# Performance work log

Measured on AMD Instinct MI355X. Metric: run time of the kernel, lower is better.

## Reference

```python
import jax, jax.numpy as jnp
import numpy as np

N_WG = 256                 # waveguides per side
N_TOTAL = N_WG * N_WG      # 65536 field points
NNZ = 16 * N_TOTAL         # ~16 couplings per waveguide (Knn-banded)
PROP_DIS = 1.0


def setup_inputs() -> dict:
    key = jax.random.key(0)
    k1, k2, k3, k4, k5 = jax.random.split(key, 5)
    row_idx = jax.random.randint(k1, (NNZ,), 0, N_TOTAL, dtype=jnp.int32)
    col_idx = jax.random.randint(k2, (NNZ,), 0, N_TOTAL, dtype=jnp.int32)
    # small coupling values so the explicit Euler scheme stays stable
    A_vals = jax.random.normal(k3, (NNZ,), dtype=jnp.float32) * 0.01
    Ur0 = jax.random.normal(k4, (N_TOTAL, 1), dtype=jnp.float32)
    Ui0 = jax.random.normal(k5, (N_TOTAL, 1), dtype=jnp.float32)
    return {"A_vals": A_vals, "row_idx": row_idx, "col_idx": col_idx,
            "Ur0": Ur0, "Ui0": Ui0, "Euler_steps": 16}


def reference(A_vals, row_idx, col_idx, Ur0, Ui0, Euler_steps):
    """Euler propagation of a complex field U under sparse coupling A:
       dU/dz = i * A @ U  ->  Ur' = Ur - dz*A@Ui ; Ui' = Ui + dz*A@Ur.
       Matches gen_Euler_with_backward_devs.forward (single device block)."""
    dz = PROP_DIS / Euler_steps

    def spmm(x):  # sparse COO matmul: [n, n] @ [n, 1]
        return jax.ops.segment_sum(A_vals[:, None] * x[col_idx], row_idx,
                                   num_segments=N_TOTAL)

    def step(carry, _):
        Ur, Ui = carry
        Ur1 = Ur - dz * spmm(Ui)
        Ui1 = Ui + dz * spmm(Ur)
        return (Ur1, Ui1), None

    (Ur, Ui), _ = jax.lax.scan(step, (Ur0, Ui0), None, length=Euler_steps)
    return Ur + 1j * Ui
```

## Files before the change

kernel.cpp:

```cpp
#include <hip/hip_runtime.h>

#define N_TOTAL 65536
#define NNZ (16 * N_TOTAL)
#define EULER_STEPS 16
#define SLOTS 48
#define TB 256
#define P 256
#define PROWS (N_TOTAL / P)
#define CHUNK 1024
#define NCHUNK (NNZ / CHUNK)
#define SCAP 24


__global__ __launch_bounds__(TB) void scatter_kernel(
    const float* __restrict__ A_vals, const int* __restrict__ row_idx,
    const int* __restrict__ col_idx, int* __restrict__ hist_t,
    uint2* __restrict__ staged) {
  __shared__ int cur[P];
  const int b = blockIdx.x, t = threadIdx.x;
  cur[t] = 0;
  __syncthreads();
  const int base = b * CHUNK;
  for (int i = t; i < CHUNK; i += TB) {
    int e = base + i;
    int r = row_idx[e];
    int p = r >> 8;
    int pos = atomicAdd(&cur[p], 1);
    if (pos < SCAP)
      staged[(size_t)(p * NCHUNK + b) * SCAP + pos] =
          make_uint2((unsigned)col_idx[e] | ((unsigned)(r & 255) << 16),
                     __float_as_uint(A_vals[e]));
  }
  __syncthreads();
  int c = cur[t];
  hist_t[t * NCHUNK + b] = (c > SCAP) ? SCAP : c;
}

__global__ __launch_bounds__(512) void build_step1_kernel(
    const uint2* __restrict__ staged, const int* __restrict__ hist_t,
    int* __restrict__ cntg, unsigned* __restrict__ entries,
    const float* __restrict__ Ur0, const float* __restrict__ Ui0,
    float2* __restrict__ Unew, float dz) {
  __shared__ unsigned ell[PROWS * SLOTS];
  __shared__ int cnt[PROWS];
  __shared__ int hcnt[NCHUNK];
  const int p = blockIdx.x, t = threadIdx.x;
  for (int i = t; i < NCHUNK; i += 512) hcnt[i] = hist_t[p * NCHUNK + i];
  for (int r = t; r < PROWS; r += 512) cnt[r] = 0;
  __syncthreads();
  for (int chunk = t; chunk < NCHUNK; chunk += 512) {
    int c = hcnt[chunk];
    const uint2* seg = staged + (size_t)(p * NCHUNK + chunk) * SCAP;
    for (int i = 0; i < c; ++i) {
      uint2 el = seg[i];
      int r = (el.x >> 16) & 255;
      int slot = atomicAdd(&cnt[r], 1);
      if (slot < SLOTS) {
        unsigned bv = el.y;
        unsigned rb = (bv + 0x7FFFu + ((bv >> 16) & 1u)) & 0xFFFF0000u;
        ell[r * SLOTS + slot] = (el.x & 0xFFFFu) | rb;
      }
    }
  }
  __syncthreads();
  const int rowbase = p * PROWS;
  for (int idx = t; idx < PROWS * SLOTS; idx += 512)
    entries[rowbase * SLOTS + idx] = ell[idx];
  for (int r = t; r < PROWS; r += 512) {
    int c = cnt[r];
    cntg[rowbase + r] = (c > SLOTS) ? SLOTS : c;
  }
  const int lr = t >> 1, l = t & 1;
  const int row = rowbase + lr;
  int c = cnt[lr];
  if (c > SLOTS) c = SLOTS;
  float sR = 0.0f, sI = 0.0f;
  for (int s = l; s < c; s += 2) {
    unsigned e = ell[lr * SLOTS + s];
    float a = __uint_as_float(e & 0xFFFF0000u);
    int col = (int)(e & 0xFFFFu);
    sR += a * Ur0[col];
    sI += a * Ui0[col];
  }
  sR += __shfl_xor(sR, 1);
  sI += __shfl_xor(sI, 1);
  if (l == 0)
    Unew[row] = make_float2(Ur0[row] - dz * sI, Ui0[row] + dz * sR);
}

__global__ __launch_bounds__(TB) void step_mid_kernel(
    const int* __restrict__ cnt, const unsigned* __restrict__ entries,
    const float2* __restrict__ Uold, float2* __restrict__ Unew, float dz) {
  int tid = blockIdx.x * blockDim.x + threadIdx.x;
  int row = tid >> 3, l = tid & 7;
  int c = cnt[row];
  if (c > SLOTS) c = SLOTS;
  const unsigned* base = entries + row * SLOTS;
  float sR = 0.0f, sI = 0.0f;
  for (int k = 2 * l; k < c; k += 16) {
    uint2 p = *(const uint2*)(base + k);
    {
      float a = __uint_as_float(p.x & 0xFFFF0000u);
      float2 u = Uold[p.x & 0xFFFFu];
      sR += a * u.x;
      sI += a * u.y;
    }
    if (k + 1 < c) {
      float a = __uint_as_float(p.y & 0xFFFF0000u);
      float2 u = Uold[p.y & 0xFFFFu];
      sR += a * u.x;
      sI += a * u.y;
    }
  }
  sR += __shfl_xor(sR, 1); sI += __shfl_xor(sI, 1);
  sR += __shfl_xor(sR, 2); sI += __shfl_xor(sI, 2);
  sR += __shfl_xor(sR, 4); sI += __shfl_xor(sI, 4);
  if (l == 0) {
    float2 u = Uold[row];
    Unew[row] = make_float2(u.x - dz * sI, u.y + dz * sR);
  }
}

__global__ __launch_bounds__(TB) void step_final_kernel(
    const int* __restrict__ cnt, const unsigned* __restrict__ entries,
    const float2* __restrict__ Uold, float* __restrict__ UrOut,
    float* __restrict__ UiOut, float dz) {
  int tid = blockIdx.x * blockDim.x + threadIdx.x;
  int row = tid >> 3, l = tid & 7;
  int c = cnt[row];
  if (c > SLOTS) c = SLOTS;
  const unsigned* base = entries + row * SLOTS;
  float sR = 0.0f, sI = 0.0f;
  for (int k = 2 * l; k < c; k += 16) {
    uint2 p = *(const uint2*)(base + k);
    {
      float a = __uint_as_float(p.x & 0xFFFF0000u);
      float2 u = Uold[p.x & 0xFFFFu];
      sR += a * u.x;
      sI += a * u.y;
    }
    if (k + 1 < c) {
      float a = __uint_as_float(p.y & 0xFFFF0000u);
      float2 u = Uold[p.y & 0xFFFFu];
      sR += a * u.x;
      sI += a * u.y;
    }
  }
  sR += __shfl_xor(sR, 1); sI += __shfl_xor(sI, 1);
  sR += __shfl_xor(sR, 2); sI += __shfl_xor(sI, 2);
  sR += __shfl_xor(sR, 4); sI += __shfl_xor(sI, 4);
  if (l == 0) {
    float2 u = Uold[row];
    UrOut[row] = u.x - dz * sI;
    UiOut[row] = u.y + dz * sR;
  }
}

extern "C" void kernel_launch(void* const* d_in, const int* in_sizes, int n_in,
                              void* d_out, int out_size, void* d_ws,
                              size_t ws_size, hipStream_t stream) {
  const float* A_vals  = (const float*)d_in[0];
  const int*   row_idx = (const int*)d_in[1];
  const int*   col_idx = (const int*)d_in[2];
  const float* Ur0     = (const float*)d_in[3];
  const float* Ui0     = (const float*)d_in[4];

  char* ws = (char*)d_ws;
  float2*   bufA    = (float2*)ws;
  float2*   bufB    = bufA + N_TOTAL;
  int*      cntg    = (int*)(bufB + N_TOTAL);
  unsigned* entries = (unsigned*)(cntg + N_TOTAL);
  int*      hist_t  = (int*)(entries + (size_t)N_TOTAL * SLOTS);
  uint2*    staged  = (uint2*)(hist_t + P * NCHUNK);

  float* UrOut = (float*)d_out;
  float* UiOut = UrOut + N_TOTAL;
  const float dz = 1.0f / (float)EULER_STEPS;
  const int gridN8 = (8 * N_TOTAL) / TB;

  scatter_kernel<<<NCHUNK, TB, 0, stream>>>(A_vals, row_idx, col_idx, hist_t,
                                            staged);
  build_step1_kernel<<<P, 512, 0, stream>>>(staged, hist_t, cntg, entries,
                                            Ur0, Ui0, bufB, dz);

  for (int s = 1; s < EULER_STEPS - 1; ++s) {
    const float2* src = (s & 1) ? bufB : bufA;
    float2*       dst = (s & 1) ? bufA : bufB;
    step_mid_kernel<<<gridN8, TB, 0, stream>>>(cntg, entries, src, dst, dz);
  }
  step_final_kernel<<<gridN8, TB, 0, stream>>>(cntg, entries, bufB, UrOut,
                                               UiOut, dz);
}
```

Measured before the change: 219.4 us.

## Fuse all stages into one persistent kernel with software grid barriers

```diff
diff --git a/kernel.cpp b/kernel.cpp
--- a/kernel.cpp
+++ b/kernel.cpp
@@ -4,53 +4,143 @@
 #define NNZ (16 * N_TOTAL)
 #define EULER_STEPS 16
 #define SLOTS 48
-#define TB 256
 #define P 256
-#define PROWS (N_TOTAL / P)
+#define PROWS 256
 #define CHUNK 1024
-#define NCHUNK (NNZ / CHUNK)
+#define NCHUNK 1024
 #define SCAP 24
 
-
-__global__ __launch_bounds__(TB) void scatter_kernel(
+#define TPB 1024
+#define NBLK 256
+#define CPB (NCHUNK / NBLK)
+#define NTHREADS (NBLK * TPB)
+#define NTASKS (8 * N_TOTAL)
+
+
+__device__ __forceinline__ float2 uload(const float2* p) {
+  unsigned long long d = __hip_atomic_load((const unsigned long long*)p,
+                                           __ATOMIC_RELAXED,
+                                           __HIP_MEMORY_SCOPE_AGENT);
+  float2 r;
+  r.x = __uint_as_float((unsigned)(d & 0xFFFFFFFFull));
+  r.y = __uint_as_float((unsigned)(d >> 32));
+  return r;
+}
+__device__ __forceinline__ void ustore(float2* p, float2 v) {
+  unsigned long long d = ((unsigned long long)__float_as_uint(v.y) << 32) |
+                         (unsigned long long)__float_as_uint(v.x);
+  __hip_atomic_store((unsigned long long*)p, d, __ATOMIC_RELAXED,
+                     __HIP_MEMORY_SCOPE_AGENT);
+}
+
+template <bool HEAVY>
+__device__ __forceinline__ void grid_barrier(int* bar) {
+  __syncthreads();
+  if (threadIdx.x == 0) {
+    if (HEAVY) __threadfence();
+    int* cnt = bar;
+    int* gen = bar + 16;
+    int g = __hip_atomic_load(gen, __ATOMIC_RELAXED, __HIP_MEMORY_SCOPE_AGENT);
+    int prev =
+        __hip_atomic_fetch_add(cnt, 1, __ATOMIC_RELAXED, __HIP_MEMORY_SCOPE_AGENT);
+    if (prev == (int)gridDim.x - 1) {
+      __hip_atomic_store(cnt, 0, __ATOMIC_RELAXED, __HIP_MEMORY_SCOPE_AGENT);
+      __hip_atomic_fetch_add(gen, 1, __ATOMIC_RELEASE, __HIP_MEMORY_SCOPE_AGENT);
+    } else {
+      while (__hip_atomic_load(gen, __ATOMIC_RELAXED,
+                               __HIP_MEMORY_SCOPE_AGENT) == g)
+        __builtin_amdgcn_s_sleep(8);
+    }
+    if (HEAVY) __threadfence();
+  }
+  __syncthreads();
+}
+
+template <bool FINAL>
+__device__ __forceinline__ void euler_step(const int* __restrict__ cntg,
+                                           const unsigned* __restrict__ entries,
+                                           const float2* __restrict__ src,
+                                           float2* __restrict__ dst,
+                                           float* __restrict__ UrOut,
+                                           float* __restrict__ UiOut, float dz,
+                                           int gtid) {
+#pragma unroll
+  for (int it = 0; it < NTASKS / NTHREADS; ++it) {
+    const int task = gtid + it * NTHREADS;
+    const int row = task >> 3;
+    const int l = task & 7;
+    const int c = cntg[row];
+    const unsigned* base = entries + row * SLOTS;
+    float sR = 0.0f, sI = 0.0f;
+    for (int k = 2 * l; k < c; k += 16) {
+      uint2 pr = *(const uint2*)(base + k);
+      {
+        float a = __uint_as_float(pr.x & 0xFFFF0000u);
+        float2 u = uload(&src[pr.x & 0xFFFFu]);
+        sR += a * u.x;
+        sI += a * u.y;
+      }
+      if (k + 1 < c) {
+        float a = __uint_as_float(pr.y & 0xFFFF0000u);
+        float2 u = uload(&src[pr.y & 0xFFFFu]);
+        sR += a * u.x;
+        sI += a * u.y;
+      }
+    }
+    sR += __shfl_xor(sR, 1); sI += __shfl_xor(sI, 1);
+    sR += __shfl_xor(sR, 2); sI += __shfl_xor(sI, 2);
+    sR += __shfl_xor(sR, 4); sI += __shfl_xor(sI, 4);
+    if (l == 0) {
+      float2 u = uload(&src[row]);
+      if (FINAL) {
+        UrOut[row] = u.x - dz * sI;
+        UiOut[row] = u.y + dz * sR;
+      } else {
+        ustore(&dst[row], make_float2(u.x - dz * sI, u.y + dz * sR));
+      }
+    }
+  }
+}
+
+__global__ __launch_bounds__(TPB, 4) void mega_kernel(
     const float* __restrict__ A_vals, const int* __restrict__ row_idx,
-    const int* __restrict__ col_idx, int* __restrict__ hist_t,
-    uint2* __restrict__ staged) {
-  __shared__ int cur[P];
-  const int b = blockIdx.x, t = threadIdx.x;
-  cur[t] = 0;
-  __syncthreads();
-  const int base = b * CHUNK;
-  for (int i = t; i < CHUNK; i += TB) {
-    int e = base + i;
-    int r = row_idx[e];
-    int p = r >> 8;
-    int pos = atomicAdd(&cur[p], 1);
-    if (pos < SCAP)
-      staged[(size_t)(p * NCHUNK + b) * SCAP + pos] =
-          make_uint2((unsigned)col_idx[e] | ((unsigned)(r & 255) << 16),
-                     __float_as_uint(A_vals[e]));
-  }
-  __syncthreads();
-  int c = cur[t];
-  hist_t[t * NCHUNK + b] = (c > SCAP) ? SCAP : c;
-}
-
-__global__ __launch_bounds__(512) void build_step1_kernel(
-    const uint2* __restrict__ staged, const int* __restrict__ hist_t,
-    int* __restrict__ cntg, unsigned* __restrict__ entries,
-    const float* __restrict__ Ur0, const float* __restrict__ Ui0,
-    float2* __restrict__ Unew, float dz) {
+    const int* __restrict__ col_idx, const float* __restrict__ Ur0,
+    const float* __restrict__ Ui0, int* __restrict__ cntg,
+    unsigned* __restrict__ entries, int* __restrict__ hist_t,
+    uint2* __restrict__ staged, float2* __restrict__ bufA,
+    float2* __restrict__ bufB, float* __restrict__ UrOut,
+    float* __restrict__ UiOut, int* bar, float dz) {
   __shared__ unsigned ell[PROWS * SLOTS];
   __shared__ int cnt[PROWS];
   __shared__ int hcnt[NCHUNK];
-  const int p = blockIdx.x, t = threadIdx.x;
-  for (int i = t; i < NCHUNK; i += 512) hcnt[i] = hist_t[p * NCHUNK + i];
-  for (int r = t; r < PROWS; r += 512) cnt[r] = 0;
-  __syncthreads();
-  for (int chunk = t; chunk < NCHUNK; chunk += 512) {
-    int c = hcnt[chunk];
-    const uint2* seg = staged + (size_t)(p * NCHUNK + chunk) * SCAP;
+  const int t = threadIdx.x;
+  const int b = blockIdx.x;
+  const int gtid = b * TPB + t;
+
+  for (int cidx = 0; cidx < CPB; ++cidx) {
+    const int chunk = b * CPB + cidx;
+    if (t < P) cnt[t] = 0;
+    __syncthreads();
+    const int e = chunk * CHUNK + t;
+    const int r = row_idx[e];
+    const int pp = r >> 8;
+    const int pos = atomicAdd(&cnt[pp], 1);
+    if (pos < SCAP)
+      staged[((size_t)pp * NCHUNK + chunk) * SCAP + pos] =
+          make_uint2((unsigned)col_idx[e] | ((unsigned)(r & 255) << 16),
+                     __float_as_uint(A_vals[e]));
+    __syncthreads();
+    if (t < P) hist_t[t * NCHUNK + chunk] = min(cnt[t], SCAP);
+    __syncthreads();
+  }
+  grid_barrier<true>(bar);
+
+  hcnt[t] = hist_t[b * NCHUNK + t];
+  if (t < PROWS) cnt[t] = 0;
+  __syncthreads();
+  {
+    const int c = hcnt[t];
+    const uint2* seg = staged + ((size_t)b * NCHUNK + t) * SCAP;
     for (int i = 0; i < c; ++i) {
       uint2 el = seg[i];
       int r = (el.x >> 16) & 255;
@@ -63,97 +153,38 @@
     }
   }
   __syncthreads();
-  const int rowbase = p * PROWS;
-  for (int idx = t; idx < PROWS * SLOTS; idx += 512)
+  const int rowbase = b * PROWS;
+  for (int idx = t; idx < PROWS * SLOTS; idx += TPB)
     entries[rowbase * SLOTS + idx] = ell[idx];
-  for (int r = t; r < PROWS; r += 512) {
-    int c = cnt[r];
-    cntg[rowbase + r] = (c > SLOTS) ? SLOTS : c;
-  }
-  const int lr = t >> 1, l = t & 1;
-  const int row = rowbase + lr;
-  int c = cnt[lr];
-  if (c > SLOTS) c = SLOTS;
-  float sR = 0.0f, sI = 0.0f;
-  for (int s = l; s < c; s += 2) {
-    unsigned e = ell[lr * SLOTS + s];
-    float a = __uint_as_float(e & 0xFFFF0000u);
-    int col = (int)(e & 0xFFFFu);
-    sR += a * Ur0[col];
-    sI += a * Ui0[col];
-  }
-  sR += __shfl_xor(sR, 1);
-  sI += __shfl_xor(sI, 1);
-  if (l == 0)
-    Unew[row] = make_float2(Ur0[row] - dz * sI, Ui0[row] + dz * sR);
-}
-
-__global__ __launch_bounds__(TB) void step_mid_kernel(
-    const int* __restrict__ cnt, const unsigned* __restrict__ entries,
-    const float2* __restrict__ Uold, float2* __restrict__ Unew, float dz) {
-  int tid = blockIdx.x * blockDim.x + threadIdx.x;
-  int row = tid >> 3, l = tid & 7;
-  int c = cnt[row];
-  if (c > SLOTS) c = SLOTS;
-  const unsigned* base = entries + row * SLOTS;
-  float sR = 0.0f, sI = 0.0f;
-  for (int k = 2 * l; k < c; k += 16) {
-    uint2 p = *(const uint2*)(base + k);
-    {
-      float a = __uint_as_float(p.x & 0xFFFF0000u);
-      float2 u = Uold[p.x & 0xFFFFu];
-      sR += a * u.x;
-      sI += a * u.y;
-    }
-    if (k + 1 < c) {
-      float a = __uint_as_float(p.y & 0xFFFF0000u);
-      float2 u = Uold[p.y & 0xFFFFu];
-      sR += a * u.x;
-      sI += a * u.y;
-    }
-  }
-  sR += __shfl_xor(sR, 1); sI += __shfl_xor(sI, 1);
-  sR += __shfl_xor(sR, 2); sI += __shfl_xor(sI, 2);
-  sR += __shfl_xor(sR, 4); sI += __shfl_xor(sI, 4);
-  if (l == 0) {
-    float2 u = Uold[row];
-    Unew[row] = make_float2(u.x - dz * sI, u.y + dz * sR);
-  }
-}
-
-__global__ __launch_bounds__(TB) void step_final_kernel(
-    const int* __restrict__ cnt, const unsigned* __restrict__ entries,
-    const float2* __restrict__ Uold, float* __restrict__ UrOut,
-    float* __restrict__ UiOut, float dz) {
-  int tid = blockIdx.x * blockDim.x + threadIdx.x;
-  int row = tid >> 3, l = tid & 7;
-  int c = cnt[row];
-  if (c > SLOTS) c = SLOTS;
-  const unsigned* base = entries + row * SLOTS;
-  float sR = 0.0f, sI = 0.0f;
-  for (int k = 2 * l; k < c; k += 16) {
-    uint2 p = *(const uint2*)(base + k);
-    {
-      float a = __uint_as_float(p.x & 0xFFFF0000u);
-      float2 u = Uold[p.x & 0xFFFFu];
-      sR += a * u.x;
-      sI += a * u.y;
-    }
-    if (k + 1 < c) {
-      float a = __uint_as_float(p.y & 0xFFFF0000u);
-      float2 u = Uold[p.y & 0xFFFFu];
-      sR += a * u.x;
-      sI += a * u.y;
-    }
-  }
-  sR += __shfl_xor(sR, 1); sI += __shfl_xor(sI, 1);
-  sR += __shfl_xor(sR, 2); sI += __shfl_xor(sI, 2);
-  sR += __shfl_xor(sR, 4); sI += __shfl_xor(sI, 4);
-  if (l == 0) {
-    float2 u = Uold[row];
-    UrOut[row] = u.x - dz * sI;
-    UiOut[row] = u.y + dz * sR;
-  }
+  if (t < PROWS) cntg[rowbase + t] = min(cnt[t], SLOTS);
+  {
+    const int lr = t >> 2, l = t & 3;
+    int c = cnt[lr];
+    if (c > SLOTS) c = SLOTS;
+    float sR = 0.0f, sI = 0.0f;
+    for (int s = l; s < c; s += 4) {
+      unsigned e = ell[lr * SLOTS + s];
+      float a = __uint_as_float(e & 0xFFFF0000u);
+      int col = (int)(e & 0xFFFFu);
+      sR += a * Ur0[col];
+      sI += a * Ui0[col];
+    }
+    sR += __shfl_xor(sR, 1); sI += __shfl_xor(sI, 1);
+    sR += __shfl_xor(sR, 2); sI += __shfl_xor(sI, 2);
+    if (l == 0) {
+      const int row = rowbase + lr;
+      ustore(&bufB[row], make_float2(Ur0[row] - dz * sI, Ui0[row] + dz * sR));
+    }
+  }
+  grid_barrier<true>(bar);
+
+  for (int s = 2; s <= EULER_STEPS - 1; ++s) {
+    const float2* src = (s & 1) ? bufA : bufB;
+    float2* dst = (s & 1) ? bufB : bufA;
+    euler_step<false>(cntg, entries, src, dst, nullptr, nullptr, dz, gtid);
+    grid_barrier<false>(bar);
+  }
+  euler_step<true>(cntg, entries, bufB, nullptr, UrOut, UiOut, dz, gtid);
 }
 
 extern "C" void kernel_launch(void* const* d_in, const int* in_sizes, int n_in,
@@ -172,22 +203,14 @@
   unsigned* entries = (unsigned*)(cntg + N_TOTAL);
   int*      hist_t  = (int*)(entries + (size_t)N_TOTAL * SLOTS);
   uint2*    staged  = (uint2*)(hist_t + P * NCHUNK);
+  int*      bar     = (int*)(staged + (size_t)P * NCHUNK * SCAP);
 
   float* UrOut = (float*)d_out;
   float* UiOut = UrOut + N_TOTAL;
   const float dz = 1.0f / (float)EULER_STEPS;
-  const int gridN8 = (8 * N_TOTAL) / TB;
-
-  scatter_kernel<<<NCHUNK, TB, 0, stream>>>(A_vals, row_idx, col_idx, hist_t,
-                                            staged);
-  build_step1_kernel<<<P, 512, 0, stream>>>(staged, hist_t, cntg, entries,
-                                            Ur0, Ui0, bufB, dz);
-
-  for (int s = 1; s < EULER_STEPS - 1; ++s) {
-    const float2* src = (s & 1) ? bufB : bufA;
-    float2*       dst = (s & 1) ? bufA : bufB;
-    step_mid_kernel<<<gridN8, TB, 0, stream>>>(cntg, entries, src, dst, dz);
-  }
-  step_final_kernel<<<gridN8, TB, 0, stream>>>(cntg, entries, bufB, UrOut,
-                                               UiOut, dz);
-}
+
+  hipMemsetAsync(bar, 0, 128, stream);
+  mega_kernel<<<NBLK, TPB, 0, stream>>>(A_vals, row_idx, col_idx, Ur0, Ui0,
+                                        cntg, entries, hist_t, staged, bufA,
+                                        bufB, UrOut, UiOut, bar, dz);
+}
```

Result: slower. 419.5 us (+91.2%).
